# Performance work log

Hardware: AMD Instinct MI355X
Metric: run time of the kernel (lower is better)

The kernel has to match this reference:

```python
import jax, jax.numpy as jnp
import numpy as np

BETA = 0.25
CODEBOOK_SIZE = 4096
DIM = 512


def setup_inputs() -> dict:
    key = jax.random.key(0)
    k1, k2 = jax.random.split(key)
    z_e = jax.random.normal(k1, (16, 1024, 512), dtype=jnp.float32)
    # kaiming_uniform-ish codebook init
    bound = float(np.sqrt(6.0 / ((1.0 + 5.0) * DIM)))
    embed = jax.random.uniform(k2, (CODEBOOK_SIZE, DIM), dtype=jnp.float32,
                               minval=-bound, maxval=bound)
    return {"z_e": z_e, "embed": embed}


def reference(z_e, embed):
    D = embed.shape[1]
    K = embed.shape[0]
    z = z_e.reshape(-1, D)                                   # [N, D]
    N = z.shape[0]
    # squared euclidean distances [N, K]
    distances = (jnp.sum(z * z, axis=1, keepdims=True)
                 - 2.0 * (z @ embed.T)
                 + jnp.sum(embed * embed, axis=1))
    indices = jnp.argmin(distances, axis=1)                  # [N]
    z_q = embed[indices].reshape(z_e.shape)                  # gather == one-hot matmul
    # straight-through estimator
    z_q_st = z_e + jax.lax.stop_gradient(z_q - z_e)
    commitment_loss = jnp.mean((jax.lax.stop_gradient(z_q) - z_e) ** 2)
    vq_loss = BETA * commitment_loss
    # avg_probs = encodings.mean(0) via histogram of indices
    counts = jnp.zeros((K,), dtype=z.dtype).at[indices].add(1.0)
    avg_probs = counts / N
    perplexity = jnp.exp(-jnp.sum(avg_probs * jnp.log(avg_probs + 1e-10)))
    return (z_q_st, indices.reshape(z_e.shape[:-1]), vq_loss, perplexity)
```

## Files before the change

kernel.cpp:

```cpp
#include <hip/hip_runtime.h>
#include <cstdint>
#include <cstddef>

typedef _Float16 f16x8 __attribute__((ext_vector_type(8)));
typedef float f32x4 __attribute__((ext_vector_type(4)));

#define NTOK 16384
#define DIMV 512
#define KCODE 4096

#define IDX_OFF (NTOK * DIMV)
#define LOSSO   (IDX_OFF + NTOK)
#define PERPO   (LOSSO + 1)

static const size_t A2_OFF = 0;
static const size_t B2_OFF = A2_OFF + (size_t)NTOK * DIMV * 2;
static const size_t EN_OFF = B2_OFF + (size_t)KCODE * DIMV * 2;
static const size_t RK_OFF = EN_OFF + (size_t)KCODE * 4;
static const size_t CNT_OFF = RK_OFF + (size_t)NTOK * 32 * 4;
static const size_t RLOSS_OFF = CNT_OFF + (size_t)KCODE * 4;

__device__ __forceinline__ float sqf(float v) {
    float p = v * v;
    asm volatile("" : "+v"(p));
    return p;
}

__device__ __forceinline__ float np_pairwise_sq(const float* xs, int t) {
    float accp = 0.0f;
    if (t < 32) {
        const float* blk = xs + (t >> 3) * 128;
        int j = t & 7;
        float rj = sqf(blk[j]);
#pragma unroll
        for (int tt = 1; tt < 16; ++tt) rj += sqf(blk[tt * 8 + j]);
        accp = rj;
    }
#pragma unroll
    for (int d = 1; d <= 16; d <<= 1) accp += __shfl_xor(accp, d, 64);
    return __shfl(accp, 0, 64);
}

__global__ void prep_k(const float* __restrict__ z, const float* __restrict__ e,
                       _Float16* __restrict__ A2, _Float16* __restrict__ B2,
                       float* __restrict__ C32, unsigned* __restrict__ counts) {
    __shared__ float es[4][512];
    const int b = blockIdx.x;
    if (b < 4096) {
        int t = b * 256 + threadIdx.x;
        int n = t >> 6;
        int dc = (t & 63) << 3;
        const float* zp = z + (size_t)n * DIMV + dc;
        float4 v0 = ((const float4*)zp)[0];
        float4 v1 = ((const float4*)zp)[1];
        float vs[8] = {v0.x, v0.y, v0.z, v0.w, v1.x, v1.y, v1.z, v1.w};
        f16x8 hi;
#pragma unroll
        for (int i = 0; i < 8; ++i) hi[i] = (_Float16)(vs[i] * 256.0f);
        *(f16x8*)(A2 + (size_t)n * DIMV + dc) = hi;
    } else {
        const int wv = threadIdx.x >> 6, t = threadIdx.x & 63;
        const int k = (b - 4096) * 4 + wv;
        const float* ep = e + (size_t)k * DIMV + t * 8;
        float4 v0 = ((const float4*)ep)[0];
        float4 v1 = ((const float4*)ep)[1];
        ((float4*)es[wv])[t * 2] = v0;
        ((float4*)es[wv])[t * 2 + 1] = v1;
        float vs[8] = {v0.x, v0.y, v0.z, v0.w, v1.x, v1.y, v1.z, v1.w};
        f16x8 hi;
#pragma unroll
        for (int i = 0; i < 8; ++i) hi[i] = (_Float16)(vs[i] * 256.0f);
        *(f16x8*)(B2 + (size_t)k * DIMV + t * 8) = hi;
        float c = np_pairwise_sq(es[wv], t);
        if (t == 0) C32[k] = c;
        if (threadIdx.x < 4) counts[(b - 4096) * 4 + threadIdx.x] = 0u;
    }
}

typedef uint32_t __attribute__((address_space(1))) gas_u32;
typedef uint32_t __attribute__((address_space(3))) las_u32;
__device__ __forceinline__ void g2l16(const _Float16* g, _Float16* l) {
    __builtin_amdgcn_global_load_lds((const gas_u32*)(uintptr_t)g,
                                     (las_u32*)(uint32_t)(uintptr_t)l, 16, 0, 0);
}

__device__ __forceinline__ void top2_merge32(unsigned& k1, unsigned& k2,
                                             unsigned o1, unsigned o2) {
    unsigned n1 = k1 < o1 ? k1 : o1;
    unsigned mx = k1 < o1 ? o1 : k1;
    unsigned n2 = k2 < o2 ? k2 : o2;
    k1 = n1;
    k2 = mx < n2 ? mx : n2;
}

#define DPP_TOP2(CTRL)                                                                     \
    {                                                                                      \
        unsigned o1 = (unsigned)__builtin_amdgcn_update_dpp(-1, (int)k1, CTRL, 0xF, 0xF, false); \
        unsigned o2 = (unsigned)__builtin_amdgcn_update_dpp(-1, (int)k2, CTRL, 0xF, 0xF, false); \
        top2_merge32(k1, k2, o1, o2);                                                      \
    }

__global__ __launch_bounds__(512) void gemm_top2_k(
    const _Float16* __restrict__ A2, const _Float16* __restrict__ B2,
    const float* __restrict__ C32, unsigned* __restrict__ rk2) {
    __shared__ _Float16 lA[128 * 64];
    __shared__ _Float16 lB[256 * 64];
    const int nt = blockIdx.x;
    const int mt = blockIdx.y;
    const int tid = threadIdx.x;
    const int w = tid >> 6, l = tid & 63;
    const int wm = w & 1, wn = w >> 1;

    const int srow = l >> 3, schunk = l & 7;
    const int gch = (schunk ^ srow) << 3;
    const _Float16* aG = A2 + (size_t)(mt * 128 + w * 16 + srow) * DIMV + gch;
    const _Float16* bG = B2 + (size_t)(nt * 256 + w * 32 + srow) * DIMV + gch;
    _Float16* aL = &lA[(w * 16) * 64];
    _Float16* bL = &lB[(w * 32) * 64];

    const int lane15 = l & 15, q = l >> 4, sx = l & 7;
    const int aRow = (wm * 64 + lane15) * 64;
    const int bRow = (wn * 64 + lane15) * 64;

    f32x4 acc[4][4] = {};

    for (int kt = 0; kt < 8; ++kt) {
        const _Float16* ag = aG + kt * 64;
        const _Float16* bg = bG + kt * 64;
#pragma unroll
        for (int r = 0; r < 2; ++r) g2l16(ag + (size_t)r * 8 * DIMV, aL + r * 512);
#pragma unroll
        for (int r = 0; r < 4; ++r) g2l16(bg + (size_t)r * 8 * DIMV, bL + r * 512);
        __syncthreads();

#pragma unroll
        for (int kk2 = 0; kk2 < 2; ++kk2) {
            f16x8 af[4], bf[4];
            const int ch = ((kk2 * 4 + q) ^ sx) << 3;
#pragma unroll
            for (int i = 0; i < 4; ++i) {
                af[i] = *(const f16x8*)&lA[aRow + i * 1024 + ch];
                bf[i] = *(const f16x8*)&lB[bRow + i * 1024 + ch];
            }
#pragma unroll
            for (int i = 0; i < 4; ++i)
#pragma unroll
                for (int j = 0; j < 4; ++j)
                    acc[i][j] = __builtin_amdgcn_mfma_f32_16x16x32_f16(af[i], bf[j], acc[i][j], 0, 0, 0);
        }
        __syncthreads();
    }

    unsigned* lk32 = (unsigned*)lA;
    const int colL = wn * 64 + lane15;
    float envals[4];
#pragma unroll
    for (int j = 0; j < 4; ++j) envals[j] = C32[nt * 256 + colL + j * 16] * 65536.0f + 4.0e6f;

#pragma unroll
    for (int i = 0; i < 4; ++i) {
#pragma unroll
        for (int rr = 0; rr < 4; ++rr) {
            unsigned k1 = 0xFFFFFFFFu, k2 = 0xFFFFFFFFu;
#pragma unroll
            for (int j = 0; j < 4; ++j) {
                float dist = envals[j] - 2.0f * acc[i][j][rr];
                unsigned key = (__float_as_uint(dist) & 0xFFFFFF00u) | (unsigned)(colL + j * 16);
                if (key < k1) { k2 = k1; k1 = key; } else if (key < k2) k2 = key;
            }
            DPP_TOP2(0x118)
            DPP_TOP2(0x114)
            DPP_TOP2(0x112)
            DPP_TOP2(0x111)
            if (lane15 == 15) {
                int rl = wm * 64 + i * 16 + q * 4 + rr;
                lk32[rl * 10 + wn * 2]     = k1;
                lk32[rl * 10 + wn * 2 + 1] = k2;
            }
        }
    }
    __syncthreads();
    if (tid < 128) {
        unsigned a1 = lk32[tid * 10], a2 = lk32[tid * 10 + 1];
#pragma unroll
        for (int p = 1; p < 4; ++p)
            top2_merge32(a1, a2, lk32[tid * 10 + p * 2], lk32[tid * 10 + p * 2 + 1]);
        size_t base = (size_t)(mt * 128 + tid) * 32 + nt * 2;
        rk2[base] = a1;
        rk2[base + 1] = a2;
    }
}

__global__ __launch_bounds__(256) void refine_k(
    const unsigned* __restrict__ rk2,
    const float* __restrict__ embed, const float* __restrict__ z,
    const float* __restrict__ C32,
    float* __restrict__ out, unsigned* __restrict__ counts,
    double* __restrict__ rloss) {
    __shared__ float zs[4][512];
    const int wv = threadIdx.x >> 6, t = threadIdx.x & 63;
    const int r = blockIdx.x * 4 + wv;
    const float4* zp = (const float4*)(z + (size_t)r * DIMV);
    float4 za = zp[t * 2], zb = zp[t * 2 + 1];
    ((float4*)zs[wv])[t * 2] = za;
    ((float4*)zs[wv])[t * 2 + 1] = zb;
    __syncthreads();

    float A32 = np_pairwise_sq(zs[wv], t);

    unsigned long long key = ~0ull;
    if (t < 32) {
        unsigned kraw = rk2[(size_t)r * 32 + t];
        unsigned col = (unsigned)(t >> 1) * 256u + (kraw & 255u);
        key = ((unsigned long long)(kraw & 0xFFFFFF00u) << 32) | col;
    }

    const int g = t >> 4, j = t & 15;
    unsigned mycand = 0;
#pragma unroll
    for (int c = 0; c < 4; ++c) {
        unsigned long long m = key;
#pragma unroll
        for (int d = 1; d < 64; d <<= 1) {
            unsigned long long o = __shfl_xor(m, d, 64);
            m = o < m ? o : m;
        }
        if (c == g) mycand = (unsigned)(m & 0xFFFFFFFFull);
        if (key == m) key = ~0ull;
    }

    const float4* ep = (const float4*)(embed + (size_t)mycand * DIMV);
    double s = 0.0;
#pragma unroll
    for (int it = 0; it < 8; ++it) {
        float4 e4 = ep[j + it * 16];
        float4 z4 = ((const float4*)zs[wv])[j + it * 16];
        s += (double)z4.x * e4.x + (double)z4.y * e4.y +
             (double)z4.z * e4.z + (double)z4.w * e4.w;
    }
#pragma unroll
    for (int d = 1; d < 16; d <<= 1) s += __shfl_xor(s, d, 64);

    float Bf = (float)s;
    float d32 = (A32 - 2.0f * Bf) + C32[mycand];
    unsigned u = __float_as_uint(d32);
    u = (u & 0x80000000u) ? ~u : (u | 0x80000000u);
    unsigned long long dk = ((unsigned long long)u << 32) | mycand;
#pragma unroll
    for (int d = 16; d < 64; d <<= 1) {
        unsigned long long o = __shfl_xor(dk, d, 64);
        dk = o < dk ? o : dk;
    }
    const unsigned ibest = (unsigned)(dk & 0xFFFFFFFFull);

    const float4* wp = (const float4*)(embed + (size_t)ibest * DIMV);
    float4 wa = wp[t * 2], wb = wp[t * 2 + 1];
    float4* op = (float4*)(out + (size_t)r * DIMV);
    op[t * 2] = wa;
    op[t * 2 + 1] = wb;
    double dx0 = (double)za.x - wa.x, dx1 = (double)za.y - wa.y;
    double dx2 = (double)za.z - wa.z, dx3 = (double)za.w - wa.w;
    double dx4 = (double)zb.x - wb.x, dx5 = (double)zb.y - wb.y;
    double dx6 = (double)zb.z - wb.z, dx7 = (double)zb.w - wb.w;
    double ls = dx0 * dx0 + dx1 * dx1 + dx2 * dx2 + dx3 * dx3 +
                dx4 * dx4 + dx5 * dx5 + dx6 * dx6 + dx7 * dx7;
#pragma unroll
    for (int d = 1; d < 64; d <<= 1) ls += __shfl_xor(ls, d, 64);
    if (t == 0) {
        out[IDX_OFF + r] = (float)ibest;
        rloss[r] = ls;
        atomicAdd(&counts[ibest], 1u);
    }
}

__global__ void scalars_k(const unsigned* __restrict__ counts,
                          const double* __restrict__ rloss, float* __restrict__ out) {
    int t = threadIdx.x;
    double ls = 0.0;
    for (int i = t; i < NTOK; i += 256) ls += rloss[i];
#pragma unroll
    for (int d = 1; d < 64; d <<= 1) ls += __shfl_xor(ls, d, 64);
    float s = 0.0f;
    for (int i = t; i < KCODE; i += 256) {
        float p = (float)counts[i] * (1.0f / (float)NTOK);
        s += p * logf(p + 1e-10f);
    }
#pragma unroll
    for (int d = 1; d < 64; d <<= 1) s += __shfl_xor(s, d, 64);
    __shared__ float red[4];
    __shared__ double redd[4];
    if ((t & 63) == 0) { red[t >> 6] = s; redd[t >> 6] = ls; }
    __syncthreads();
    if (t == 0) {
        float tot = red[0] + red[1] + red[2] + red[3];
        double ltot = redd[0] + redd[1] + redd[2] + redd[3];
        out[PERPO] = expf(-tot);
        out[LOSSO] = 0.25f * (float)(ltot * (1.0 / (double)(NTOK * DIMV)));
    }
}

extern "C" void kernel_launch(void* const* d_in, const int* in_sizes, int n_in,
                              void* d_out, int out_size, void* d_ws, size_t ws_size,
                              hipStream_t stream) {
    const float* z     = (const float*)d_in[0];
    const float* embed = (const float*)d_in[1];
    float* out = (float*)d_out;
    char* ws = (char*)d_ws;

    _Float16* A2 = (_Float16*)(ws + A2_OFF);
    _Float16* B2 = (_Float16*)(ws + B2_OFF);
    float* C32 = (float*)(ws + EN_OFF);
    unsigned* rk2 = (unsigned*)(ws + RK_OFF);
    unsigned* counts = (unsigned*)(ws + CNT_OFF);
    double* rloss = (double*)(ws + RLOSS_OFF);

    prep_k<<<5120, 256, 0, stream>>>(z, embed, A2, B2, C32, counts);
    gemm_top2_k<<<dim3(16, 128), 512, 0, stream>>>(A2, B2, C32, rk2);
    refine_k<<<NTOK / 4, 256, 0, stream>>>(rk2, embed, z, C32, out, counts, rloss);
    scalars_k<<<1, 256, 0, stream>>>(counts, rloss, out);
}
```

Baseline: 221.7 us.

## Fuse scalar reduction into refine kernel via last-block atomics and reuse codebook rows

The separate scalars kernel is removed. Each refine block atomically adds its loss into one of 64 double partial slots and bumps a completion counter, and the last block to finish computes perplexity and loss. The winning candidate's codebook row, already loaded for the distance refinement, is staged through shared memory instead of being re-read from global memory. This saves a kernel launch and a global re-fetch, at the cost of atomics, thread fences and extra block-wide barriers in every block.

```diff
diff --git a/kernel.cpp b/kernel.cpp
--- a/kernel.cpp
+++ b/kernel.cpp
@@ -18,7 +18,8 @@
 static const size_t EN_OFF = B2_OFF + (size_t)KCODE * DIMV * 2;
 static const size_t RK_OFF = EN_OFF + (size_t)KCODE * 4;
 static const size_t CNT_OFF = RK_OFF + (size_t)NTOK * 32 * 4;
-static const size_t RLOSS_OFF = CNT_OFF + (size_t)KCODE * 4;
+static const size_t LP_OFF  = CNT_OFF + (size_t)KCODE * 4;
+static const size_t DONE_OFF = LP_OFF + 64 * 8;
 
 __device__ __forceinline__ float sqf(float v) {
     float p = v * v;
@@ -43,7 +44,8 @@
 
 __global__ void prep_k(const float* __restrict__ z, const float* __restrict__ e,
                        _Float16* __restrict__ A2, _Float16* __restrict__ B2,
-                       float* __restrict__ C32, unsigned* __restrict__ counts) {
+                       float* __restrict__ C32, unsigned* __restrict__ counts,
+                       double* __restrict__ lossPart, unsigned* __restrict__ done) {
     __shared__ float es[4][512];
     const int b = blockIdx.x;
     if (b < 4096) {
@@ -74,6 +76,10 @@
         float c = np_pairwise_sq(es[wv], t);
         if (t == 0) C32[k] = c;
         if (threadIdx.x < 4) counts[(b - 4096) * 4 + threadIdx.x] = 0u;
+        if (b == 4096) {
+            if (threadIdx.x < 64) lossPart[threadIdx.x] = 0.0;
+            if (threadIdx.x == 64) *done = 0u;
+        }
     }
 }
 
@@ -196,8 +202,11 @@
     const float* __restrict__ embed, const float* __restrict__ z,
     const float* __restrict__ C32,
     float* __restrict__ out, unsigned* __restrict__ counts,
-    double* __restrict__ rloss) {
+    double* __restrict__ lossPart, unsigned* __restrict__ done) {
     __shared__ float zs[4][512];
+    __shared__ float zqs[4][512];
+    __shared__ double lsh[4];
+    __shared__ unsigned oldsh;
     const int wv = threadIdx.x >> 6, t = threadIdx.x & 63;
     const int r = blockIdx.x * 4 + wv;
     const float4* zp = (const float4*)(z + (size_t)r * DIMV);
@@ -230,10 +239,12 @@
     }
 
     const float4* ep = (const float4*)(embed + (size_t)mycand * DIMV);
+    float4 ev[8];
     double s = 0.0;
 #pragma unroll
     for (int it = 0; it < 8; ++it) {
         float4 e4 = ep[j + it * 16];
+        ev[it] = e4;
         float4 z4 = ((const float4*)zs[wv])[j + it * 16];
         s += (double)z4.x * e4.x + (double)z4.y * e4.y +
              (double)z4.z * e4.z + (double)z4.w * e4.w;
@@ -253,8 +264,14 @@
     }
     const unsigned ibest = (unsigned)(dk & 0xFFFFFFFFull);
 
-    const float4* wp = (const float4*)(embed + (size_t)ibest * DIMV);
-    float4 wa = wp[t * 2], wb = wp[t * 2 + 1];
+    if (mycand == ibest) {
+#pragma unroll
+        for (int it = 0; it < 8; ++it) ((float4*)zqs[wv])[j + it * 16] = ev[it];
+    }
+    __syncthreads();
+
+    float4 wa = ((const float4*)zqs[wv])[t * 2];
+    float4 wb = ((const float4*)zqs[wv])[t * 2 + 1];
     float4* op = (float4*)(out + (size_t)r * DIMV);
     op[t * 2] = wa;
     op[t * 2 + 1] = wb;
@@ -268,34 +285,43 @@
     for (int d = 1; d < 64; d <<= 1) ls += __shfl_xor(ls, d, 64);
     if (t == 0) {
         out[IDX_OFF + r] = (float)ibest;
-        rloss[r] = ls;
+        lsh[wv] = ls;
         atomicAdd(&counts[ibest], 1u);
-    }
-}
-
-__global__ void scalars_k(const unsigned* __restrict__ counts,
-                          const double* __restrict__ rloss, float* __restrict__ out) {
-    int t = threadIdx.x;
-    double ls = 0.0;
-    for (int i = t; i < NTOK; i += 256) ls += rloss[i];
-#pragma unroll
-    for (int d = 1; d < 64; d <<= 1) ls += __shfl_xor(ls, d, 64);
-    float s = 0.0f;
-    for (int i = t; i < KCODE; i += 256) {
-        float p = (float)counts[i] * (1.0f / (float)NTOK);
-        s += p * logf(p + 1e-10f);
-    }
-#pragma unroll
-    for (int d = 1; d < 64; d <<= 1) s += __shfl_xor(s, d, 64);
-    __shared__ float red[4];
-    __shared__ double redd[4];
-    if ((t & 63) == 0) { red[t >> 6] = s; redd[t >> 6] = ls; }
-    __syncthreads();
-    if (t == 0) {
-        float tot = red[0] + red[1] + red[2] + red[3];
-        double ltot = redd[0] + redd[1] + redd[2] + redd[3];
-        out[PERPO] = expf(-tot);
-        out[LOSSO] = 0.25f * (float)(ltot * (1.0 / (double)(NTOK * DIMV)));
+        __threadfence();
+    }
+    __syncthreads();
+    if (threadIdx.x == 0) {
+        double bsum = lsh[0] + lsh[1] + lsh[2] + lsh[3];
+        atomicAdd(&lossPart[blockIdx.x & 63], bsum);
+        __threadfence();
+        oldsh = atomicAdd(done, 1u);
+    }
+    __syncthreads();
+
+    if (oldsh == 4095u) {
+        __threadfence();
+        int tt = threadIdx.x;
+        double lt = (tt < 64) ? atomicAdd(&lossPart[tt], 0.0) : 0.0;
+#pragma unroll
+        for (int d = 1; d < 64; d <<= 1) lt += __shfl_xor(lt, d, 64);
+        float sent = 0.0f;
+        for (int i = tt; i < KCODE; i += 256) {
+            unsigned c = atomicAdd(&counts[i], 0u);
+            float p = (float)c * (1.0f / (float)NTOK);
+            sent += p * logf(p + 1e-10f);
+        }
+#pragma unroll
+        for (int d = 1; d < 64; d <<= 1) sent += __shfl_xor(sent, d, 64);
+        __shared__ float fred[4];
+        __shared__ double dred[4];
+        if ((tt & 63) == 0) { fred[tt >> 6] = sent; dred[tt >> 6] = lt; }
+        __syncthreads();
+        if (tt == 0) {
+            float stot = fred[0] + fred[1] + fred[2] + fred[3];
+            double ltot = dred[0];
+            out[PERPO] = expf(-stot);
+            out[LOSSO] = 0.25f * (float)(ltot * (1.0 / (double)(NTOK * DIMV)));
+        }
     }
 }
 
@@ -312,10 +338,10 @@
     float* C32 = (float*)(ws + EN_OFF);
     unsigned* rk2 = (unsigned*)(ws + RK_OFF);
     unsigned* counts = (unsigned*)(ws + CNT_OFF);
-    double* rloss = (double*)(ws + RLOSS_OFF);
-
-    prep_k<<<5120, 256, 0, stream>>>(z, embed, A2, B2, C32, counts);
+    double* lossPart = (double*)(ws + LP_OFF);
+    unsigned* done = (unsigned*)(ws + DONE_OFF);
+
+    prep_k<<<5120, 256, 0, stream>>>(z, embed, A2, B2, C32, counts, lossPart, done);
     gemm_top2_k<<<dim3(16, 128), 512, 0, stream>>>(A2, B2, C32, rk2);
-    refine_k<<<NTOK / 4, 256, 0, stream>>>(rk2, embed, z, C32, out, counts, rloss);
-    scalars_k<<<1, 256, 0, stream>>>(counts, rloss, out);
-}
+    refine_k<<<NTOK / 4, 256, 0, stream>>>(rk2, embed, z, C32, out, counts, lossPart, done);
+}
```

Measured after the change: 784.2 us. +253.7%, slower.
